# Kernel tuning notes

Measured on AMD Instinct MI355X. Metric: run time of the kernel, lower is better.

The kernel has to match this reference:

```python
import jax, jax.numpy as jnp
import numpy as np

B, M, Q, D = 32, 8192, 64, 128

def setup_inputs() -> dict:
    key = jax.random.key(0)
    k1, k2, k3, k4 = jax.random.split(key, 4)
    story_a = jax.random.normal(k1, (B, M, D), dtype=jnp.float32)
    u = jax.random.normal(k2, (B, Q, D), dtype=jnp.float32)
    story_c = jax.random.normal(k3, (B, M, D), dtype=jnp.float32)
    H = jax.random.normal(k4, (D, D), dtype=jnp.float32) * (1.0 / np.sqrt(D))
    return {"story_a": story_a, "u": u, "story_c": story_c, "H": H}

def reference(story_a, u, story_c, H):
    # scores: Dot(axes=-1)([story_a, u]) -> (B, M, Q)
    m = jnp.einsum('bmd,bqd->bmq', story_a, u)
    # Keras Softmax() default axis=-1: normalize over Q (faithful to original)
    p = jax.nn.softmax(m, axis=-1)          # (B, M, Q)
    p = jnp.swapaxes(p, 1, 2)                # (B, Q, M)
    # output memory: Dot(axes=(2,1))([p, story_c]) -> (B, Q, D)
    c = jnp.einsum('bqm,bmd->bqd', p, story_c)
    # linear residual: K.dot(u, H) + c
    mapped_u = jnp.einsum('bqd,de->bqe', u, H)
    return c + mapped_u
```

## Files before the change

### kernel.cpp

```cpp
#include <hip/hip_runtime.h>

#define B_ 32
#define M_ 8192
#define Q_ 64
#define D_ 128
#define MT 64
#define NT 16
#define CHN 8
#define LDP 72
#define SA 268
#define SC 260
#define AW (8 * SA)
#define CW (8 * SC)
#define WBUF (AW + CW)

typedef __attribute__((ext_vector_type(8))) short short8;
typedef __attribute__((ext_vector_type(4))) float floatx4;

__device__ __forceinline__ unsigned pkbf(float a, float b) {
  unsigned ua = __builtin_bit_cast(unsigned, a) + 0x8000u;
  unsigned ub = __builtin_bit_cast(unsigned, b) + 0x8000u;
  return __builtin_amdgcn_perm(ub, ua, 0x07060302u);
}

__device__ __forceinline__ short8 pack8(float4 a, float4 b) {
  union { unsigned u[4]; short8 v; } o;
  o.u[0] = pkbf(a.x, a.y); o.u[1] = pkbf(a.z, a.w);
  o.u[2] = pkbf(b.x, b.y); o.u[3] = pkbf(b.z, b.w);
  return o.v;
}

template <int CTRL>
__device__ __forceinline__ float dppadd(float x) {
  int y = __builtin_amdgcn_update_dpp(0, __builtin_bit_cast(int, x), CTRL, 0xF, 0xF, true);
  return x + __builtin_bit_cast(float, y);
}
__device__ __forceinline__ float rowsum16(float x) {
  x = dppadd<0x128>(x); x = dppadd<0x124>(x);
  x = dppadd<0x122>(x); x = dppadd<0x121>(x);
  return x;
}

__device__ __forceinline__ void barrier_lds() {
  asm volatile("s_waitcnt lgkmcnt(0)\n\ts_barrier" ::: "memory");
}

__device__ __forceinline__ void dma16(const float* g, float* l) {
  __builtin_amdgcn_global_load_lds(
      (const __attribute__((address_space(1))) void*)g,
      (__attribute__((address_space(3))) void*)l, 16, 0, 0);
}

template <bool ATOMIC>
__global__ __launch_bounds__(256, 1) void memn2n_main(
    const float* __restrict__ A, const float* __restrict__ U,
    const float* __restrict__ Cc, float* __restrict__ dst) {
  __shared__ __align__(16) float sMem[4 * 2 * WBUF];
  __shared__ __align__(16) unsigned short sP[2][Q_ * LDP];

  const int tid  = threadIdx.x;
  const int lane = tid & 63;
  const int w    = tid >> 6;
  const int l15  = lane & 15;
  const int quad = (lane >> 4) & 3;

  const int blk = blockIdx.x;
  const int b   = blk / CHN;
  const int ch  = blk - b * CHN;

  const float* Abase = A + ((size_t)b * M_ + (size_t)ch * NT * MT) * D_;
  const float* Cbase = Cc + ((size_t)b * M_ + (size_t)ch * NT * MT) * D_;

  float* const wbase = sMem + w * (2 * WBUF);

  const float* ub = U + (size_t)b * Q_ * D_;
  short8 uf[4][4];
#pragma unroll
  for (int qs = 0; qs < 4; ++qs)
#pragma unroll
    for (int ks = 0; ks < 4; ++ks) {
      const float* p = ub + (16 * qs + l15) * D_ + 32 * ks + 8 * quad;
      uf[qs][ks] = pack8(*(const float4*)p, *(const float4*)(p + 4));
    }

#define DMA_TILE(tt, bufp)                                                       \
  {                                                                              \
    const float* At_ = Abase + ((size_t)(tt) * MT + 16 * w) * D_;                \
    const float* Ct_ = Cbase + (size_t)(tt) * MT * D_ + 32 * w;                  \
    float* dA_ = (bufp);                                                         \
    float* dC_ = (bufp) + AW;                                                    \
    _Pragma("unroll") for (int j = 0; j < 8; ++j)                                \
      dma16(At_ + j * 256 + lane * 4, dA_ + j * SA);                             \
    _Pragma("unroll") for (int j = 0; j < 8; ++j)                                \
      dma16(Ct_ + (8 * j + (lane >> 3)) * D_ + (lane & 7) * 4, dC_ + j * SC);    \
  }

  floatx4 acc[2][4];
#pragma unroll
  for (int i = 0; i < 2; ++i)
#pragma unroll
    for (int j = 0; j < 4; ++j) acc[i][j] = (floatx4){0.f, 0.f, 0.f, 0.f};

  DMA_TILE(0, wbase);

  for (int t = 0; t < NT; ++t) {
    float* buf = wbase + (t & 1) * WBUF;

    if (t + 1 < NT) {
      float* nbuf = wbase + ((t + 1) & 1) * WBUF;
      DMA_TILE(t + 1, nbuf);
      asm volatile("s_waitcnt vmcnt(16)" ::: "memory");
    } else {
      asm volatile("s_waitcnt vmcnt(0)" ::: "memory");
    }

    floatx4 s1[4];
#pragma unroll
    for (int qs = 0; qs < 4; ++qs) s1[qs] = (floatx4){0.f, 0.f, 0.f, 0.f};
    {
      const int rb = (l15 >> 1) * SA + (l15 & 1) * 128 + 8 * quad;
#pragma unroll
      for (int ks = 0; ks < 4; ++ks) {
        float4 x = *(const float4*)(buf + rb + 32 * ks);
        float4 y = *(const float4*)(buf + rb + 32 * ks + 4);
        short8 af = pack8(x, y);
#pragma unroll
        for (int qs = 0; qs < 4; ++qs)
          s1[qs] = __builtin_amdgcn_mfma_f32_16x16x32_bf16(af, uf[qs][ks], s1[qs], 0, 0, 0);
      }
    }

    float pv[4][4];
#pragma unroll
    for (int rg = 0; rg < 4; ++rg) {
      const float c = 1.4426950408889634f;
      float e0 = exp2f(s1[0][rg] * c), e1 = exp2f(s1[1][rg] * c);
      float e2 = exp2f(s1[2][rg] * c), e3 = exp2f(s1[3][rg] * c);
      float sm = (e0 + e1) + (e2 + e3);
      sm = rowsum16(sm);
      float inv = __builtin_amdgcn_rcpf(sm);
      pv[0][rg] = e0 * inv; pv[1][rg] = e1 * inv;
      pv[2][rg] = e2 * inv; pv[3][rg] = e3 * inv;
    }

    unsigned short* sPt = &sP[t & 1][0];
#pragma unroll
    for (int qs = 0; qs < 4; ++qs)
      *(uint2*)&sPt[(16 * qs + l15) * LDP + 16 * w + 4 * quad] =
          make_uint2(pkbf(pv[qs][0], pv[qs][1]), pkbf(pv[qs][2], pv[qs][3]));

    barrier_lds();

    const float* aC = buf + AW;
#pragma unroll
    for (int ks = 0; ks < 2; ++ks) {
      short8 pa[4];
#pragma unroll
      for (int qs = 0; qs < 4; ++qs)
        pa[qs] = *(const short8*)&sPt[(16 * qs + l15) * LDP + 32 * ks + 8 * quad];
#pragma unroll
      for (int ds = 0; ds < 2; ++ds) {
        float cc[8];
#pragma unroll
        for (int j = 0; j < 8; ++j)
          cc[j] = aC[(4 * ks + quad) * SC + j * 32 + 16 * ds + l15];
        union { unsigned u[4]; short8 v; } o;
        o.u[0] = pkbf(cc[0], cc[1]); o.u[1] = pkbf(cc[2], cc[3]);
        o.u[2] = pkbf(cc[4], cc[5]); o.u[3] = pkbf(cc[6], cc[7]);
#pragma unroll
        for (int qs = 0; qs < 4; ++qs)
          acc[ds][qs] = __builtin_amdgcn_mfma_f32_16x16x32_bf16(pa[qs], o.v, acc[ds][qs], 0, 0, 0);
      }
    }
  }

  if (ATOMIC) {
#pragma unroll
    for (int ds = 0; ds < 2; ++ds)
#pragma unroll
      for (int qs = 0; qs < 4; ++qs)
#pragma unroll
        for (int rg = 0; rg < 4; ++rg) {
          int q = qs * 16 + quad * 4 + rg;
          int d = l15 + 16 * (2 * w + ds);
          atomicAdd(&dst[((size_t)b * Q_ + q) * D_ + d], acc[ds][qs][rg]);
        }
  } else {
    float* pp = dst + (((size_t)ch * B_ + b) * Q_) * D_;
#pragma unroll
    for (int ds = 0; ds < 2; ++ds)
#pragma unroll
      for (int qs = 0; qs < 4; ++qs)
#pragma unroll
        for (int rg = 0; rg < 4; ++rg) {
          int q = qs * 16 + quad * 4 + rg;
          int d = l15 + 16 * (2 * w + ds);
          pp[q * D_ + d] = acc[ds][qs][rg];
        }
  }
#undef DMA_TILE
}

__global__ __launch_bounds__(128) void memn2n_reduce(
    const float* __restrict__ U, const float* __restrict__ H,
    const float* __restrict__ part, float* __restrict__ out, int chunks) {
  int bq = blockIdx.x;
  int b = bq >> 6, q = bq & 63;
  int d = threadIdx.x;
  __shared__ float su[D_];
  size_t row = ((size_t)b * Q_ + q) * D_;
  su[d] = U[row + d];
  __syncthreads();
  float acc = 0.f;
#pragma unroll 16
  for (int e = 0; e < D_; ++e) acc = fmaf(su[e], H[e * D_ + d], acc);
#pragma unroll 8
  for (int ch = 0; ch < chunks; ++ch)
    acc += part[(((size_t)ch * B_ + b) * Q_ + q) * D_ + d];
  out[row + d] = acc;
}

extern "C" void kernel_launch(void* const* d_in, const int* in_sizes, int n_in,
                              void* d_out, int out_size, void* d_ws, size_t ws_size,
                              hipStream_t stream) {
  const float* A  = (const float*)d_in[0];
  const float* U  = (const float*)d_in[1];
  const float* Cc = (const float*)d_in[2];
  const float* H  = (const float*)d_in[3];
  float* out = (float*)d_out;

  size_t part_bytes = (size_t)CHN * B_ * Q_ * D_ * sizeof(float);
  if (ws_size >= part_bytes) {
    float* part = (float*)d_ws;
    memn2n_main<false><<<B_ * CHN, 256, 0, stream>>>(A, U, Cc, part);
    memn2n_reduce<<<B_ * Q_, 128, 0, stream>>>(U, H, part, out, CHN);
  } else {
    memn2n_reduce<<<B_ * Q_, 128, 0, stream>>>(U, H, nullptr, out, 0);
    memn2n_main<true><<<B_ * CHN, 256, 0, stream>>>(A, U, Cc, out);
  }
}
```

Before: 295.7 us.

## Replace LDS DMA staging with register prefetch and double the chunk count

Drops the global_load_lds double-buffered staging of A and C tiles. Each lane now prefetches its own A and C fragments for the next tile straight into registers. U is converted to bf16 once and held in LDS instead of registers. CHN goes from 8 to 16 and launch bounds allow 2 blocks per CU, aiming for more occupancy and parallelism with far less LDS. In exchange, the C loads become scalar strided global reads, register pressure rises, and the reduce kernel has twice as many partial sums to add.

```diff
diff --git a/kernel.cpp b/kernel.cpp
--- a/kernel.cpp
+++ b/kernel.cpp
@@ -5,14 +5,10 @@
 #define Q_ 64
 #define D_ 128
 #define MT 64
-#define NT 16
-#define CHN 8
+#define CHN 16
+#define NT (M_ / (CHN * MT))
 #define LDP 72
-#define SA 268
-#define SC 260
-#define AW (8 * SA)
-#define CW (8 * SC)
-#define WBUF (AW + CW)
+#define LDU 136
 
 typedef __attribute__((ext_vector_type(8))) short short8;
 typedef __attribute__((ext_vector_type(4))) float floatx4;
@@ -45,17 +41,11 @@
   asm volatile("s_waitcnt lgkmcnt(0)\n\ts_barrier" ::: "memory");
 }
 
-__device__ __forceinline__ void dma16(const float* g, float* l) {
-  __builtin_amdgcn_global_load_lds(
-      (const __attribute__((address_space(1))) void*)g,
-      (__attribute__((address_space(3))) void*)l, 16, 0, 0);
-}
-
 template <bool ATOMIC>
-__global__ __launch_bounds__(256, 1) void memn2n_main(
+__global__ __launch_bounds__(256, 2) void memn2n_main(
     const float* __restrict__ A, const float* __restrict__ U,
     const float* __restrict__ Cc, float* __restrict__ dst) {
-  __shared__ __align__(16) float sMem[4 * 2 * WBUF];
+  __shared__ __align__(16) unsigned short sU[Q_ * LDU];
   __shared__ __align__(16) unsigned short sP[2][Q_ * LDP];
 
   const int tid  = threadIdx.x;
@@ -71,29 +61,37 @@
   const float* Abase = A + ((size_t)b * M_ + (size_t)ch * NT * MT) * D_;
   const float* Cbase = Cc + ((size_t)b * M_ + (size_t)ch * NT * MT) * D_;
 
-  float* const wbase = sMem + w * (2 * WBUF);
-
-  const float* ub = U + (size_t)b * Q_ * D_;
-  short8 uf[4][4];
-#pragma unroll
-  for (int qs = 0; qs < 4; ++qs)
-#pragma unroll
-    for (int ks = 0; ks < 4; ++ks) {
-      const float* p = ub + (16 * qs + l15) * D_ + 32 * ks + 8 * quad;
-      uf[qs][ks] = pack8(*(const float4*)p, *(const float4*)(p + 4));
-    }
-
-#define DMA_TILE(tt, bufp)                                                       \
-  {                                                                              \
-    const float* At_ = Abase + ((size_t)(tt) * MT + 16 * w) * D_;                \
-    const float* Ct_ = Cbase + (size_t)(tt) * MT * D_ + 32 * w;                  \
-    float* dA_ = (bufp);                                                         \
-    float* dC_ = (bufp) + AW;                                                    \
-    _Pragma("unroll") for (int j = 0; j < 8; ++j)                                \
-      dma16(At_ + j * 256 + lane * 4, dA_ + j * SA);                             \
-    _Pragma("unroll") for (int j = 0; j < 8; ++j)                                \
-      dma16(Ct_ + (8 * j + (lane >> 3)) * D_ + (lane & 7) * 4, dC_ + j * SC);    \
-  }
+  {
+    const float* ub = U + (size_t)b * Q_ * D_;
+#pragma unroll
+    for (int i = 0; i < 8; ++i) {
+      int idx = tid + i * 256;
+      int q = idx >> 5, c4 = idx & 31;
+      float4 v = *(const float4*)(ub + q * D_ + c4 * 4);
+      *(uint2*)&sU[q * LDU + c4 * 4] = make_uint2(pkbf(v.x, v.y), pkbf(v.z, v.w));
+    }
+  }
+
+  const float* Ap = Abase + ((size_t)(16 * w + l15) * D_ + 8 * quad);
+  const float* Cp = Cbase + (size_t)(8 * quad) * D_ + 32 * w + l15;
+
+  float4 a_st[8];
+  float  c_st[32];
+
+#pragma unroll
+  for (int ks = 0; ks < 4; ++ks) {
+    a_st[2 * ks]     = *(const float4*)(Ap + 32 * ks);
+    a_st[2 * ks + 1] = *(const float4*)(Ap + 32 * ks + 4);
+  }
+#pragma unroll
+  for (int ks = 0; ks < 2; ++ks)
+#pragma unroll
+    for (int ds = 0; ds < 2; ++ds)
+#pragma unroll
+      for (int j = 0; j < 8; ++j)
+        c_st[(2 * ks + ds) * 8 + j] = Cp[(size_t)(32 * ks + j) * D_ + 16 * ds];
+
+  barrier_lds();
 
   floatx4 acc[2][4];
 #pragma unroll
@@ -101,34 +99,30 @@
 #pragma unroll
     for (int j = 0; j < 4; ++j) acc[i][j] = (floatx4){0.f, 0.f, 0.f, 0.f};
 
-  DMA_TILE(0, wbase);
-
   for (int t = 0; t < NT; ++t) {
-    float* buf = wbase + (t & 1) * WBUF;
+    short8 af[4];
+#pragma unroll
+    for (int ks = 0; ks < 4; ++ks) af[ks] = pack8(a_st[2 * ks], a_st[2 * ks + 1]);
 
     if (t + 1 < NT) {
-      float* nbuf = wbase + ((t + 1) & 1) * WBUF;
-      DMA_TILE(t + 1, nbuf);
-      asm volatile("s_waitcnt vmcnt(16)" ::: "memory");
-    } else {
-      asm volatile("s_waitcnt vmcnt(0)" ::: "memory");
+      const float* An = Ap + (size_t)(t + 1) * MT * D_;
+#pragma unroll
+      for (int ks = 0; ks < 4; ++ks) {
+        a_st[2 * ks]     = *(const float4*)(An + 32 * ks);
+        a_st[2 * ks + 1] = *(const float4*)(An + 32 * ks + 4);
+      }
     }
 
     floatx4 s1[4];
 #pragma unroll
     for (int qs = 0; qs < 4; ++qs) s1[qs] = (floatx4){0.f, 0.f, 0.f, 0.f};
-    {
-      const int rb = (l15 >> 1) * SA + (l15 & 1) * 128 + 8 * quad;
-#pragma unroll
-      for (int ks = 0; ks < 4; ++ks) {
-        float4 x = *(const float4*)(buf + rb + 32 * ks);
-        float4 y = *(const float4*)(buf + rb + 32 * ks + 4);
-        short8 af = pack8(x, y);
-#pragma unroll
-        for (int qs = 0; qs < 4; ++qs)
-          s1[qs] = __builtin_amdgcn_mfma_f32_16x16x32_bf16(af, uf[qs][ks], s1[qs], 0, 0, 0);
+#pragma unroll
+    for (int ks = 0; ks < 4; ++ks)
+#pragma unroll
+      for (int qs = 0; qs < 4; ++qs) {
+        short8 uq = *(const short8*)&sU[(16 * qs + l15) * LDU + 32 * ks + 8 * quad];
+        s1[qs] = __builtin_amdgcn_mfma_f32_16x16x32_bf16(af[ks], uq, s1[qs], 0, 0, 0);
       }
-    }
 
     float pv[4][4];
 #pragma unroll
@@ -151,26 +145,41 @@
 
     barrier_lds();
 
-    const float* aC = buf + AW;
-#pragma unroll
-    for (int ks = 0; ks < 2; ++ks) {
-      short8 pa[4];
-#pragma unroll
-      for (int qs = 0; qs < 4; ++qs)
-        pa[qs] = *(const short8*)&sPt[(16 * qs + l15) * LDP + 32 * ks + 8 * quad];
+    short8 cf[4];
+#pragma unroll
+    for (int ks = 0; ks < 2; ++ks)
 #pragma unroll
       for (int ds = 0; ds < 2; ++ds) {
-        float cc[8];
-#pragma unroll
-        for (int j = 0; j < 8; ++j)
-          cc[j] = aC[(4 * ks + quad) * SC + j * 32 + 16 * ds + l15];
+        const float* cc = &c_st[(2 * ks + ds) * 8];
         union { unsigned u[4]; short8 v; } o;
         o.u[0] = pkbf(cc[0], cc[1]); o.u[1] = pkbf(cc[2], cc[3]);
         o.u[2] = pkbf(cc[4], cc[5]); o.u[3] = pkbf(cc[6], cc[7]);
+        cf[2 * ks + ds] = o.v;
+      }
+
+    if (t + 1 < NT) {
+      const float* Cn = Cp + (size_t)(t + 1) * MT * D_;
+#pragma unroll
+      for (int ks = 0; ks < 2; ++ks)
+#pragma unroll
+        for (int ds = 0; ds < 2; ++ds)
+#pragma unroll
+          for (int j = 0; j < 8; ++j)
+            c_st[(2 * ks + ds) * 8 + j] = Cn[(size_t)(32 * ks + j) * D_ + 16 * ds];
+    }
+
+#pragma unroll
+    for (int ks = 0; ks < 2; ++ks) {
+      short8 pa[4];
+#pragma unroll
+      for (int qs = 0; qs < 4; ++qs)
+        pa[qs] = *(const short8*)&sPt[(16 * qs + l15) * LDP + 32 * ks + 8 * quad];
+#pragma unroll
+      for (int ds = 0; ds < 2; ++ds)
 #pragma unroll
         for (int qs = 0; qs < 4; ++qs)
-          acc[ds][qs] = __builtin_amdgcn_mfma_f32_16x16x32_bf16(pa[qs], o.v, acc[ds][qs], 0, 0, 0);
-      }
+          acc[ds][qs] =
+              __builtin_amdgcn_mfma_f32_16x16x32_bf16(pa[qs], cf[2 * ks + ds], acc[ds][qs], 0, 0, 0);
     }
   }
 
@@ -198,7 +207,6 @@
           pp[q * D_ + d] = acc[ds][qs][rg];
         }
   }
-#undef DMA_TILE
 }
 
 __global__ __launch_bounds__(128) void memn2n_reduce(
```

Measured after the change: 291.6 us. No clear change (-1.4%).
